# Performance work log

Measured on AMD Instinct MI355X. Metric: run time of the kernel, lower is better.

## Reference

```python
import jax, jax.numpy as jnp
import numpy as np

N = 50000
E = 800000
IN_DIM = 128
HID = 32
HEADS = 4
NEG_SLOPE = 0.2


def setup_inputs() -> dict:
    key = jax.random.key(0)
    ks = jax.random.split(key, 12)
    x = jax.random.normal(ks[0], (N, IN_DIM), dtype=jnp.float32)
    edge_index = jax.random.randint(ks[1], (2, E), 0, N, dtype=jnp.int64)
    s1 = 1.0 / np.sqrt(IN_DIM)
    s2 = 1.0 / np.sqrt(HEADS * HID)
    W1 = jax.random.normal(ks[2], (IN_DIM, HEADS * HID), dtype=jnp.float32) * s1
    a_src1 = jax.random.normal(ks[3], (HEADS, HID), dtype=jnp.float32) * s1
    a_dst1 = jax.random.normal(ks[4], (HEADS, HID), dtype=jnp.float32) * s1
    b1 = jnp.zeros((HEADS * HID,), dtype=jnp.float32)
    W2 = jax.random.normal(ks[5], (HEADS * HID, HID), dtype=jnp.float32) * s2
    a_src2 = jax.random.normal(ks[6], (1, HID), dtype=jnp.float32) * s2
    a_dst2 = jax.random.normal(ks[7], (1, HID), dtype=jnp.float32) * s2
    b2 = jnp.zeros((HID,), dtype=jnp.float32)
    return {"x": x, "edge_index": edge_index, "W1": W1, "a_src1": a_src1,
            "a_dst1": a_dst1, "b1": b1, "W2": W2, "a_src2": a_src2,
            "a_dst2": a_dst2, "b2": b2}


def _gat_layer(x, W, a_src, a_dst, bias, src, dst, heads, ch):
    n = x.shape[0]
    h = (x @ W).reshape(n, heads, ch)                    # [N,H,C]
    # per-node attention halves (GATv1): a_src . h_i, a_dst . h_j
    al_s = jnp.einsum('nhc,hc->nh', h, a_src)            # [N,H]
    al_d = jnp.einsum('nhc,hc->nh', h, a_dst)
    e = jax.nn.leaky_relu(al_s[src] + al_d[dst], NEG_SLOPE)  # [E,H]
    # segment softmax over edges sharing the same destination
    e_max = jax.ops.segment_max(e, dst, num_segments=n)
    e_exp = jnp.exp(e - e_max[dst])
    denom = jax.ops.segment_sum(e_exp, dst, num_segments=n)
    alpha = e_exp / (denom[dst] + 1e-16)                 # [E,H]
    msg = h[src] * alpha[:, :, None]                     # [E,H,C]
    out = jax.ops.segment_sum(msg, dst, num_segments=n)  # [N,H,C]
    return out.reshape(n, heads * ch) + bias


def reference(x, edge_index, W1, a_src1, a_dst1, b1, W2, a_src2, a_dst2, b2):
    n = x.shape[0]
    # PyG GATConv adds self-loops by default
    loops = jnp.arange(n, dtype=edge_index.dtype)
    src = jnp.concatenate([edge_index[0], loops])
    dst = jnp.concatenate([edge_index[1], loops])
    h = _gat_layer(x, W1, a_src1, a_dst1, b1, src, dst, HEADS, HID)
    h = jax.nn.elu(h)
    out = _gat_layer(h, W2, a_src2, a_dst2, b2, src, dst, 1, HID)
    return out
```

## Files before the change

### kernel.cpp

```cpp
#include <hip/hip_runtime.h>
#include <hip/hip_bf16.h>

#define NN 50000
#define EE 800000
#define EN (EE + NN)
#define IN_DIM 128
#define HID 32
#define HEADS 4
#define F1 (HEADS * HID)
#define NEG 0.2f
#define SLOT 64
#define CPAD 16

typedef __hip_bfloat16 bf16;
typedef __bf16 bf16x8 __attribute__((ext_vector_type(8)));
typedef float f32x4 __attribute__((ext_vector_type(4)));

__device__ __forceinline__ float cvt(float v) { return v; }
__device__ __forceinline__ float cvt(bf16 v)  { return __bfloat162float(v); }

__device__ __forceinline__ float bflo(unsigned u) {
    union { unsigned u; float f; } v; v.u = u << 16; return v.f;
}
__device__ __forceinline__ float bfhi(unsigned u) {
    union { unsigned u; float f; } v; v.u = u & 0xFFFF0000u; return v.f;
}

__device__ __forceinline__ unsigned short f2bf_bits(float f) {
    union { float f; unsigned u; } v; v.f = f;
    unsigned r = v.u + 0x7FFFu + ((v.u >> 16) & 1u);
    return (unsigned short)(r >> 16);
}

__device__ __forceinline__ unsigned short f2h_bits(float f) {
    _Float16 h = (_Float16)f;
    union { _Float16 h; unsigned short s; } v; v.h = h; return v.s;
}
__device__ __forceinline__ float h2f(unsigned short s) {
    union { _Float16 h; unsigned short s; } v; v.s = s; return (float)v.h;
}

#define ZERO_B ((NN * CPAD + 255) / 256)
#define PREP_B (1 + ZERO_B + 16 + 1)

__global__ void k_prep(const void* xv, const void* eiv,
                       const void* W1v, const void* W2v,
                       int* __restrict__ flags, int* __restrict__ counts,
                       unsigned short* __restrict__ W1T,
                       unsigned short* __restrict__ W2T) {
    const int b = blockIdx.x, t = threadIdx.x;
    if (b == 0) {
        if (t < 64) {
            const unsigned* xw = (const unsigned*)xv;
            const unsigned* ew = (const unsigned*)eiv;
            int lo_nz = 0, huge = 0, hi_nz = 0;
            for (int j = 0; j < 4; ++j) {
                unsigned w = xw[t * 4 + j];
                unsigned lo = w & 0xFFFFu;
                if (lo != 0u) lo_nz = 1;
                if (((lo >> 7) & 0xFFu) >= 0xC0u) huge = 1;
                unsigned eo = ew[(t * 4 + j) * 2 + 1];
                if (eo != 0u) hi_nz = 1;
            }
            unsigned long long m_lo = __ballot(lo_nz);
            unsigned long long m_hg = __ballot(huge);
            unsigned long long m_hi = __ballot(hi_nz);
            if (t == 0) {
                flags[0] = (m_lo == 0ull || m_hg != 0ull) ? 1 : 0;
                flags[1] = (m_hi == 0ull) ? 1 : 0;
            }
        }
        return;
    }
    if (b <= ZERO_B) {
        int i = (b - 1) * 256 + t;
        if (i < NN * CPAD) counts[i] = 0;
        return;
    }
    __shared__ int sf;
    if (t < 64) {
        const unsigned* xw = (const unsigned*)xv;
        int lo_nz = 0, huge = 0;
        for (int j = 0; j < 4; ++j) {
            unsigned w = xw[t * 4 + j];
            unsigned lo = w & 0xFFFFu;
            if (lo != 0u) lo_nz = 1;
            if (((lo >> 7) & 0xFFu) >= 0xC0u) huge = 1;
        }
        unsigned long long m_lo = __ballot(lo_nz);
        unsigned long long m_hg = __ballot(huge);
        if (t == 0) sf = (m_lo == 0ull || m_hg != 0ull) ? 1 : 0;
    }
    __syncthreads();
    const int f32in = sf;
    const int tb = b - 1 - ZERO_B;
    if (tb < 16) {
        const unsigned short* wg = (const unsigned short*)W1v;
        const float* wf = (const float*)W1v;
        for (int i = 0; i < 4; ++i) {
            int j = tb * 1024 + i * 256 + t;
            int k = j >> 7, n = j & 127;
            W1T[n * 128 + k] = f32in ? f2bf_bits(wf[j]) : wg[j];
        }
    } else {
        const unsigned short* wg = (const unsigned short*)W2v;
        const float* wf = (const float*)W2v;
        for (int i = 0; i < 16; ++i) {
            int j = i * 256 + t;
            int k = j >> 5, n = j & 31;
            W2T[n * 128 + k] = f32in ? f2bf_bits(wf[j]) : wg[j];
        }
    }
}

#define PAIR_B ((EN / 2 + 255) / 256)

__global__ void k_hist(const void* ei, const int* __restrict__ flags,
                       int* __restrict__ counts, int* __restrict__ sr) {
    int p = blockIdx.x * 256 + threadIdx.x;
    int i2 = p * 2;
    if (i2 >= EN) return;
    int s0, s1, d0, d1;
    if (i2 >= EE) { s0 = d0 = i2 - EE; s1 = d1 = s0 + 1; }
    else if (flags[1]) {
        const long long* e64 = (const long long*)ei;
        long2 ss = *(const long2*)&e64[i2];
        long2 dd = *(const long2*)&e64[EE + i2];
        s0 = (int)ss.x; s1 = (int)ss.y; d0 = (int)dd.x; d1 = (int)dd.y;
    } else {
        const int* e32 = (const int*)ei;
        int2 ss = *(const int2*)&e32[i2];
        int2 dd = *(const int2*)&e32[EE + i2];
        s0 = ss.x; s1 = ss.y; d0 = dd.x; d1 = dd.y;
    }
    int r0 = atomicAdd(&counts[d0 * CPAD], 1);
    int r1 = atomicAdd(&counts[d1 * CPAD], 1);
    int slot0 = (r0 < SLOT) ? d0 * SLOT + r0 : -1;
    int slot1 = (r1 < SLOT) ? d1 * SLOT + r1 : -1;
    *(int4*)&sr[i2 * 2] = make_int4(slot0, s0, slot1, s1);
}

#define MROWS 64
#define LDK 136
#define LIN_B ((NN + MROWS - 1) / MROWS)
#define FUSE_B (LIN_B + PAIR_B)

__global__ __launch_bounds__(256) void k_fused(
    const void* xv, const unsigned short* __restrict__ W1T,
    const void* as1v, const void* ad1v,
    const int* __restrict__ flags, const int* __restrict__ sr,
    int* __restrict__ srcs2, unsigned* __restrict__ h1,
    float* __restrict__ als, float* __restrict__ ald)
{
    if (blockIdx.x >= LIN_B) {
        int p = (blockIdx.x - LIN_B) * 256 + threadIdx.x;
        int i2 = p * 2;
        if (i2 >= EN) return;
        int4 v = *(const int4*)&sr[i2 * 2];
        if (v.x >= 0) srcs2[v.x] = v.y;
        if (v.z >= 0) srcs2[v.z] = v.w;
        return;
    }

    __shared__ __align__(16) char smem[(MROWS + 128) * LDK * 2];
    unsigned short* xs  = (unsigned short*)smem;
    unsigned short* w1t = xs + MROWS * LDK;
    float* hs = (float*)smem;
    __shared__ float sa[F1], sd[F1];

    const int t = threadIdx.x;
    const int row0 = blockIdx.x * MROWS;
    const int f32in = flags[0];

    if (t < F1) {
        sa[t] = f32in ? ((const float*)as1v)[t] : cvt(((const bf16*)as1v)[t]);
        sd[t] = f32in ? ((const float*)ad1v)[t] : cvt(((const bf16*)ad1v)[t]);
    }
    if (!f32in) {
        const uint4* xg = (const uint4*)xv;
        for (int i = 0; i < 4; ++i) {
            int id = i * 256 + t;
            int m = id >> 4, seg = id & 15;
            int gr = row0 + m;
            uint4 val = (gr < NN) ? xg[(size_t)gr * 16 + seg] : make_uint4(0, 0, 0, 0);
            *(uint4*)&xs[m * LDK + seg * 8] = val;
        }
    } else {
        const float4* xf = (const float4*)xv;
        for (int i = 0; i < 8; ++i) {
            int id = i * 256 + t;
            int m = id >> 5, c = id & 31;
            int gr = row0 + m;
            float4 v = (gr < NN) ? xf[(size_t)gr * 32 + c]
                                 : make_float4(0.f, 0.f, 0.f, 0.f);
            unsigned w0 = (unsigned)f2bf_bits(v.x) | ((unsigned)f2bf_bits(v.y) << 16);
            unsigned w1 = (unsigned)f2bf_bits(v.z) | ((unsigned)f2bf_bits(v.w) << 16);
            *(uint2*)&xs[m * LDK + c * 4] = make_uint2(w0, w1);
        }
    }
    {
        const uint4* wg = (const uint4*)W1T;
        for (int i = 0; i < 8; ++i) {
            int id = i * 256 + t;
            int n = id >> 4, seg = id & 15;
            *(uint4*)&w1t[n * LDK + seg * 8] = wg[id];
        }
    }
    __syncthreads();

    const int wave = t >> 6, lane = t & 63, quad = lane >> 4, l16 = lane & 15;
    f32x4 acc[8];
#pragma unroll
    for (int ni = 0; ni < 8; ++ni) acc[ni] = (f32x4){0.f, 0.f, 0.f, 0.f};

    const int arow = wave * 16 + l16;
#pragma unroll
    for (int kc = 0; kc < 4; ++kc) {
        int ko = kc * 32 + quad * 8;
        bf16x8 av = *(const bf16x8*)&xs[arow * LDK + ko];
#pragma unroll
        for (int ni = 0; ni < 8; ++ni) {
            bf16x8 bv = *(const bf16x8*)&w1t[(ni * 16 + l16) * LDK + ko];
            acc[ni] = __builtin_amdgcn_mfma_f32_16x16x32_bf16(av, bv, acc[ni], 0, 0, 0);
        }
    }
    __syncthreads();

#pragma unroll
    for (int ni = 0; ni < 8; ++ni)
#pragma unroll
        for (int r = 0; r < 4; ++r) {
            int m = wave * 16 + quad * 4 + r;
            hs[m * 132 + ni * 16 + l16] = acc[ni][r];
        }
    __syncthreads();

    for (int i = 0; i < 16; ++i) {
        int id = i * 256 + t;
        int m = id >> 6, wd = id & 63;
        int gr = row0 + m;
        if (gr < NN) {
            unsigned pw = (unsigned)f2bf_bits(hs[m * 132 + 2 * wd]) |
                          ((unsigned)f2bf_bits(hs[m * 132 + 2 * wd + 1]) << 16);
            h1[(size_t)gr * 64 + wd] = pw;
        }
    }
    {
        int m = t >> 2, h = t & 3;
        int gr = row0 + m;
        if (gr < NN) {
            float ps = 0.f, pd = 0.f;
#pragma unroll
            for (int jj = 0; jj < 32; ++jj) {
                int j = (jj + 8 * h) & 31;
                float v = hs[m * 132 + h * 32 + j];
                ps += v * sa[h * 32 + j];
                pd += v * sd[h * 32 + j];
            }
            als[gr * 4 + h] = ps;
            ald[gr * 4 + h] = pd;
        }
    }
}

__global__ __launch_bounds__(256) void k_agg1(
    const int* __restrict__ counts, const int* __restrict__ srcs2,
    const float* __restrict__ als, const float* __restrict__ ald,
    const bf16* __restrict__ h1, const void* b1v, const int* __restrict__ flags,
    uint4* __restrict__ hm)
{
    const int lane = threadIdx.x & 63;
    const int d = blockIdx.x * 4 + (threadIdx.x >> 6);
    const int q = lane >> 4;
    const int u = lane & 15;
    const int h = u >> 2;
    const int start = d * SLOT;
    const int end = start + min(counts[d * CPAD], SLOT);
    const uint4* rows = (const uint4*)h1;
    const float advh = ald[d * 4 + h];

    float A[8] = {0,0,0,0,0,0,0,0}, B[8] = {0,0,0,0,0,0,0,0};
    float DA = 0.f, DB = 0.f;
    int e = start + q;
    for (; e + 4 < end; e += 8) {
        int s0 = srcs2[e], s1 = srcs2[e + 4];
        float e0 = als[s0 * 4 + h] + advh;
        float e1 = als[s1 * 4 + h] + advh;
        e0 = e0 > 0.f ? e0 : NEG * e0;
        e1 = e1 > 0.f ? e1 : NEG * e1;
        float x0 = __expf(e0), x1 = __expf(e1);
        uint4 u0 = rows[(size_t)s0 * 16 + u];
        uint4 u1 = rows[(size_t)s1 * 16 + u];
        A[0] += x0 * bflo(u0.x); A[1] += x0 * bfhi(u0.x);
        A[2] += x0 * bflo(u0.y); A[3] += x0 * bfhi(u0.y);
        A[4] += x0 * bflo(u0.z); A[5] += x0 * bfhi(u0.z);
        A[6] += x0 * bflo(u0.w); A[7] += x0 * bfhi(u0.w); DA += x0;
        B[0] += x1 * bflo(u1.x); B[1] += x1 * bfhi(u1.x);
        B[2] += x1 * bflo(u1.y); B[3] += x1 * bfhi(u1.y);
        B[4] += x1 * bflo(u1.z); B[5] += x1 * bfhi(u1.z);
        B[6] += x1 * bflo(u1.w); B[7] += x1 * bfhi(u1.w); DB += x1;
    }
    for (; e < end; e += 4) {
        int s0 = srcs2[e];
        float e0 = als[s0 * 4 + h] + advh;
        e0 = e0 > 0.f ? e0 : NEG * e0;
        float x0 = __expf(e0);
        uint4 u0 = rows[(size_t)s0 * 16 + u];
        A[0] += x0 * bflo(u0.x); A[1] += x0 * bfhi(u0.x);
        A[2] += x0 * bflo(u0.y); A[3] += x0 * bfhi(u0.y);
        A[4] += x0 * bflo(u0.z); A[5] += x0 * bfhi(u0.z);
        A[6] += x0 * bflo(u0.w); A[7] += x0 * bfhi(u0.w); DA += x0;
    }
    float a[8];
#pragma unroll
    for (int j = 0; j < 8; ++j) a[j] = A[j] + B[j];
    float dsum = DA + DB;
#pragma unroll
    for (int j = 0; j < 8; ++j) {
        a[j] += __shfl_xor(a[j], 16);
        a[j] += __shfl_xor(a[j], 32);
    }
    dsum += __shfl_xor(dsum, 16);
    dsum += __shfl_xor(dsum, 32);
    if (q == 0) {
        float inv = 1.f / (dsum + 1e-16f);
        float bb[8];
        if (flags[0]) {
            float4 b0 = ((const float4*)b1v)[2 * u];
            float4 b1 = ((const float4*)b1v)[2 * u + 1];
            bb[0] = b0.x; bb[1] = b0.y; bb[2] = b0.z; bb[3] = b0.w;
            bb[4] = b1.x; bb[5] = b1.y; bb[6] = b1.z; bb[7] = b1.w;
        } else {
            uint4 ub = ((const uint4*)b1v)[u];
            bb[0] = bflo(ub.x); bb[1] = bfhi(ub.x); bb[2] = bflo(ub.y); bb[3] = bfhi(ub.y);
            bb[4] = bflo(ub.z); bb[5] = bfhi(ub.z); bb[6] = bflo(ub.w); bb[7] = bfhi(ub.w);
        }
        float v[8];
#pragma unroll
        for (int j = 0; j < 8; ++j) {
            float vv = a[j] * inv + bb[j];
            v[j] = vv > 0.f ? vv : (__expf(vv) - 1.f);
        }
        uint4 w;
        w.x = (unsigned)f2bf_bits(v[0]) | ((unsigned)f2bf_bits(v[1]) << 16);
        w.y = (unsigned)f2bf_bits(v[2]) | ((unsigned)f2bf_bits(v[3]) << 16);
        w.z = (unsigned)f2bf_bits(v[4]) | ((unsigned)f2bf_bits(v[5]) << 16);
        w.w = (unsigned)f2bf_bits(v[6]) | ((unsigned)f2bf_bits(v[7]) << 16);
        hm[(size_t)d * 16 + u] = w;
    }
}

__global__ __launch_bounds__(256) void k_mid_mfma(
    const bf16* __restrict__ hm, const unsigned short* __restrict__ W2T,
    const void* as2v, const void* ad2v,
    const int* __restrict__ flags, unsigned short* __restrict__ h2,
    float* __restrict__ als2, float* __restrict__ ald2)
{
    __shared__ __align__(16) unsigned short hs[MROWS * LDK];
    __shared__ __align__(16) unsigned short w2t[32 * LDK];
    __shared__ float sa2[HID], sd2[HID];

    const int t = threadIdx.x;
    const int row0 = blockIdx.x * MROWS;
    const int f32in = flags[0];

    if (t < HID) {
        sa2[t] = f32in ? ((const float*)as2v)[t] : cvt(((const bf16*)as2v)[t]);
        sd2[t] = f32in ? ((const float*)ad2v)[t] : cvt(((const bf16*)ad2v)[t]);
    }
    {
        const uint4* hg = (const uint4*)hm;
        for (int i = 0; i < 4; ++i) {
            int id = i * 256 + t;
            int m = id >> 4, seg = id & 15;
            int gr = row0 + m;
            uint4 val = (gr < NN) ? hg[(size_t)gr * 16 + seg] : make_uint4(0, 0, 0, 0);
            *(uint4*)&hs[m * LDK + seg * 8] = val;
        }
        const uint4* wg = (const uint4*)W2T;
        for (int i = 0; i < 2; ++i) {
            int id = i * 256 + t;
            int n = id >> 4, seg = id & 15;
            *(uint4*)&w2t[n * LDK + seg * 8] = wg[id];
        }
    }
    __syncthreads();

    const int wave = t >> 6, lane = t & 63, quad = lane >> 4, l16 = lane & 15;
    f32x4 acc[2];
    acc[0] = (f32x4){0.f, 0.f, 0.f, 0.f};
    acc[1] = (f32x4){0.f, 0.f, 0.f, 0.f};
    const int arow = wave * 16 + l16;
#pragma unroll
    for (int kc = 0; kc < 4; ++kc) {
        int ko = kc * 32 + quad * 8;
        bf16x8 av = *(const bf16x8*)&hs[arow * LDK + ko];
#pragma unroll
        for (int ni = 0; ni < 2; ++ni) {
            bf16x8 bv = *(const bf16x8*)&w2t[(ni * 16 + l16) * LDK + ko];
            acc[ni] = __builtin_amdgcn_mfma_f32_16x16x32_bf16(av, bv, acc[ni], 0, 0, 0);
        }
    }

#pragma unroll
    for (int ni = 0; ni < 2; ++ni)
#pragma unroll
        for (int r = 0; r < 4; ++r) {
            int gr = row0 + wave * 16 + quad * 4 + r;
            if (gr < NN) h2[(size_t)gr * 32 + ni * 16 + l16] = f2h_bits(acc[ni][r]);
        }

    float ps[4], pd[4];
#pragma unroll
    for (int r = 0; r < 4; ++r) {
        ps[r] = acc[0][r] * sa2[l16] + acc[1][r] * sa2[16 + l16];
        pd[r] = acc[0][r] * sd2[l16] + acc[1][r] * sd2[16 + l16];
    }
#pragma unroll
    for (int mask = 1; mask < 16; mask <<= 1)
#pragma unroll
        for (int r = 0; r < 4; ++r) {
            ps[r] += __shfl_xor(ps[r], mask);
            pd[r] += __shfl_xor(pd[r], mask);
        }
    if (l16 == 0) {
#pragma unroll
        for (int r = 0; r < 4; ++r) {
            int gr = row0 + wave * 16 + quad * 4 + r;
            if (gr < NN) { als2[gr] = ps[r]; ald2[gr] = pd[r]; }
        }
    }
}

__global__ __launch_bounds__(256) void k_agg2(
    const int* __restrict__ counts, const int* __restrict__ srcs2,
    const float* __restrict__ als2, const float* __restrict__ ald2,
    const uint2* __restrict__ h2,
    const void* b2v, const int* __restrict__ flags, void* out)
{
    const int lane = threadIdx.x & 63;
    const int node = blockIdx.x * 4 + (threadIdx.x >> 6);
    const int q = lane >> 3;
    const int u = lane & 7;
    const int start = node * SLOT;
    const int end = start + min(counts[node * CPAD], SLOT);
    const float adv = ald2[node];

    float A0 = 0.f, A1 = 0.f, A2 = 0.f, A3 = 0.f, D0 = 0.f;
    for (int e = start + q; e < end; e += 8) {
        int s0 = srcs2[e];
        float e0 = als2[s0] + adv;
        e0 = e0 > 0.f ? e0 : NEG * e0;
        float x0 = __expf(e0);
        uint2 w = h2[(size_t)s0 * 8 + u];
        A0 += x0 * h2f((unsigned short)(w.x & 0xFFFFu));
        A1 += x0 * h2f((unsigned short)(w.x >> 16));
        A2 += x0 * h2f((unsigned short)(w.y & 0xFFFFu));
        A3 += x0 * h2f((unsigned short)(w.y >> 16));
        D0 += x0;
    }
    A0 += __shfl_xor(A0, 8);  A1 += __shfl_xor(A1, 8);
    A2 += __shfl_xor(A2, 8);  A3 += __shfl_xor(A3, 8);  D0 += __shfl_xor(D0, 8);
    A0 += __shfl_xor(A0, 16); A1 += __shfl_xor(A1, 16);
    A2 += __shfl_xor(A2, 16); A3 += __shfl_xor(A3, 16); D0 += __shfl_xor(D0, 16);
    A0 += __shfl_xor(A0, 32); A1 += __shfl_xor(A1, 32);
    A2 += __shfl_xor(A2, 32); A3 += __shfl_xor(A3, 32); D0 += __shfl_xor(D0, 32);
    if (q == 0) {
        float inv = 1.f / (D0 + 1e-16f);
        float r0 = A0 * inv, r1 = A1 * inv, r2 = A2 * inv, r3 = A3 * inv;
        if (flags[0]) {
            float4 bb = ((const float4*)b2v)[u];
            ((float4*)out)[(size_t)node * 8 + u] =
                make_float4(r0 + bb.x, r1 + bb.y, r2 + bb.z, r3 + bb.w);
        } else {
            uint2 ub = ((const uint2*)b2v)[u];
            r0 += bflo(ub.x); r1 += bfhi(ub.x); r2 += bflo(ub.y); r3 += bfhi(ub.y);
            unsigned w0 = (unsigned)f2bf_bits(r0) | ((unsigned)f2bf_bits(r1) << 16);
            unsigned w1 = (unsigned)f2bf_bits(r2) | ((unsigned)f2bf_bits(r3) << 16);
            ((uint2*)out)[(size_t)node * 8 + u] = make_uint2(w0, w1);
        }
    }
}

extern "C" void kernel_launch(void* const* d_in, const int* in_sizes, int n_in,
                              void* d_out, int out_size, void* d_ws, size_t ws_size,
                              hipStream_t stream) {
    const void* x    = d_in[0];
    const void* ei   = d_in[1];
    const void* W1   = d_in[2];
    const void* a_s1 = d_in[3];
    const void* a_d1 = d_in[4];
    const void* b1   = d_in[5];
    const void* W2   = d_in[6];
    const void* a_s2 = d_in[7];
    const void* a_d2 = d_in[8];
    const void* b2v  = d_in[9];

    int*   flags  = (int*)d_ws;
    char*  pc     = (char*)d_ws + 256;
    uint4* hm     = (uint4*)pc;            pc += (size_t)NN * 16 * 16;
    int*   sr     = (int*)hm;
    bf16*  h1     = (bf16*)pc;             pc += (size_t)NN * F1 * 2;
    unsigned short* h2 = (unsigned short*)h1;
    int*   srcs2  = (int*)pc;              pc += (size_t)NN * SLOT * 4;
    float* al_s1  = (float*)pc;            pc += (size_t)NN * HEADS * 4;
    float* al_d1  = (float*)pc;            pc += (size_t)NN * HEADS * 4;
    float* al_s2  = (float*)pc;            pc += (size_t)NN * 4;
    float* al_d2  = (float*)pc;            pc += (size_t)NN * 4;
    int*   counts = (int*)pc;              pc += (size_t)NN * CPAD * 4;
    unsigned short* W1T = (unsigned short*)pc; pc += (size_t)128 * 128 * 2;
    unsigned short* W2T = (unsigned short*)pc; pc += (size_t)32 * 128 * 2;

    k_prep<<<PREP_B, 256, 0, stream>>>(x, ei, W1, W2, flags, counts, W1T, W2T);
    k_hist<<<PAIR_B, 256, 0, stream>>>(ei, flags, counts, sr);
    k_fused<<<FUSE_B, 256, 0, stream>>>(x, W1T, a_s1, a_d1, flags, sr, srcs2,
                                        (unsigned*)h1, al_s1, al_d1);
    k_agg1<<<NN / 4, 256, 0, stream>>>(counts, srcs2, al_s1, al_d1, h1, b1,
                                       flags, hm);
    k_mid_mfma<<<(NN + MROWS - 1) / MROWS, 256, 0, stream>>>((const bf16*)hm, W2T, a_s2,
                                                             a_d2, flags, h2, al_s2, al_d2);
    k_agg2<<<NN / 4, 256, 0, stream>>>(counts, srcs2, al_s2, al_d2,
                                       (const uint2*)h2, b2v, flags, d_out);
}
```

Measured before the change: 214.7 us.

## Fuse layer-2 linear projection and attention logits into layer-1 aggregation kernel

Removes the separate MFMA mid kernel. After each wave finishes aggregating a node's layer-1 features and applying bias and ELU, it stages the 128-wide row in shared memory and computes the 32-wide W2 projection with scalar FMAs, plus the layer-2 attention logits. This avoids writing and re-reading the intermediate hm buffer and saves a launch. In exchange, every wave reloads W2T from cache and does non-tensor-core math, and the workspace layout changes so h2 and sr no longer alias.

```diff
diff --git a/kernel.cpp b/kernel.cpp
--- a/kernel.cpp
+++ b/kernel.cpp
@@ -266,11 +266,17 @@
 __global__ __launch_bounds__(256) void k_agg1(
     const int* __restrict__ counts, const int* __restrict__ srcs2,
     const float* __restrict__ als, const float* __restrict__ ald,
-    const bf16* __restrict__ h1, const void* b1v, const int* __restrict__ flags,
-    uint4* __restrict__ hm)
+    const bf16* __restrict__ h1, const void* b1v,
+    const unsigned short* __restrict__ W2T,
+    const void* as2v, const void* ad2v,
+    const int* __restrict__ flags,
+    unsigned short* __restrict__ h2,
+    float* __restrict__ als2, float* __restrict__ ald2)
 {
+    __shared__ float hmrow[4][128];
     const int lane = threadIdx.x & 63;
-    const int d = blockIdx.x * 4 + (threadIdx.x >> 6);
+    const int wave = threadIdx.x >> 6;
+    const int d = blockIdx.x * 4 + wave;
     const int q = lane >> 4;
     const int u = lane & 15;
     const int h = u >> 2;
@@ -322,114 +328,54 @@
     }
     dsum += __shfl_xor(dsum, 16);
     dsum += __shfl_xor(dsum, 32);
+
+    float inv = 1.f / (dsum + 1e-16f);
+    float bb[8];
+    if (flags[0]) {
+        float4 b0 = ((const float4*)b1v)[2 * u];
+        float4 b1 = ((const float4*)b1v)[2 * u + 1];
+        bb[0] = b0.x; bb[1] = b0.y; bb[2] = b0.z; bb[3] = b0.w;
+        bb[4] = b1.x; bb[5] = b1.y; bb[6] = b1.z; bb[7] = b1.w;
+    } else {
+        uint4 ub = ((const uint4*)b1v)[u];
+        bb[0] = bflo(ub.x); bb[1] = bfhi(ub.x); bb[2] = bflo(ub.y); bb[3] = bfhi(ub.y);
+        bb[4] = bflo(ub.z); bb[5] = bfhi(ub.z); bb[6] = bflo(ub.w); bb[7] = bfhi(ub.w);
+    }
+    float v[8];
+#pragma unroll
+    for (int j = 0; j < 8; ++j) {
+        float vv = a[j] * inv + bb[j];
+        v[j] = vv > 0.f ? vv : (__expf(vv) - 1.f);
+    }
     if (q == 0) {
-        float inv = 1.f / (dsum + 1e-16f);
-        float bb[8];
-        if (flags[0]) {
-            float4 b0 = ((const float4*)b1v)[2 * u];
-            float4 b1 = ((const float4*)b1v)[2 * u + 1];
-            bb[0] = b0.x; bb[1] = b0.y; bb[2] = b0.z; bb[3] = b0.w;
-            bb[4] = b1.x; bb[5] = b1.y; bb[6] = b1.z; bb[7] = b1.w;
-        } else {
-            uint4 ub = ((const uint4*)b1v)[u];
-            bb[0] = bflo(ub.x); bb[1] = bfhi(ub.x); bb[2] = bflo(ub.y); bb[3] = bfhi(ub.y);
-            bb[4] = bflo(ub.z); bb[5] = bfhi(ub.z); bb[6] = bflo(ub.w); bb[7] = bfhi(ub.w);
-        }
-        float v[8];
-#pragma unroll
-        for (int j = 0; j < 8; ++j) {
-            float vv = a[j] * inv + bb[j];
-            v[j] = vv > 0.f ? vv : (__expf(vv) - 1.f);
-        }
-        uint4 w;
-        w.x = (unsigned)f2bf_bits(v[0]) | ((unsigned)f2bf_bits(v[1]) << 16);
-        w.y = (unsigned)f2bf_bits(v[2]) | ((unsigned)f2bf_bits(v[3]) << 16);
-        w.z = (unsigned)f2bf_bits(v[4]) | ((unsigned)f2bf_bits(v[5]) << 16);
-        w.w = (unsigned)f2bf_bits(v[6]) | ((unsigned)f2bf_bits(v[7]) << 16);
-        hm[(size_t)d * 16 + u] = w;
-    }
-}
-
-__global__ __launch_bounds__(256) void k_mid_mfma(
-    const bf16* __restrict__ hm, const unsigned short* __restrict__ W2T,
-    const void* as2v, const void* ad2v,
-    const int* __restrict__ flags, unsigned short* __restrict__ h2,
-    float* __restrict__ als2, float* __restrict__ ald2)
-{
-    __shared__ __align__(16) unsigned short hs[MROWS * LDK];
-    __shared__ __align__(16) unsigned short w2t[32 * LDK];
-    __shared__ float sa2[HID], sd2[HID];
-
-    const int t = threadIdx.x;
-    const int row0 = blockIdx.x * MROWS;
-    const int f32in = flags[0];
-
-    if (t < HID) {
-        sa2[t] = f32in ? ((const float*)as2v)[t] : cvt(((const bf16*)as2v)[t]);
-        sd2[t] = f32in ? ((const float*)ad2v)[t] : cvt(((const bf16*)ad2v)[t]);
-    }
-    {
-        const uint4* hg = (const uint4*)hm;
-        for (int i = 0; i < 4; ++i) {
-            int id = i * 256 + t;
-            int m = id >> 4, seg = id & 15;
-            int gr = row0 + m;
-            uint4 val = (gr < NN) ? hg[(size_t)gr * 16 + seg] : make_uint4(0, 0, 0, 0);
-            *(uint4*)&hs[m * LDK + seg * 8] = val;
-        }
-        const uint4* wg = (const uint4*)W2T;
-        for (int i = 0; i < 2; ++i) {
-            int id = i * 256 + t;
-            int n = id >> 4, seg = id & 15;
-            *(uint4*)&w2t[n * LDK + seg * 8] = wg[id];
-        }
-    }
-    __syncthreads();
-
-    const int wave = t >> 6, lane = t & 63, quad = lane >> 4, l16 = lane & 15;
-    f32x4 acc[2];
-    acc[0] = (f32x4){0.f, 0.f, 0.f, 0.f};
-    acc[1] = (f32x4){0.f, 0.f, 0.f, 0.f};
-    const int arow = wave * 16 + l16;
-#pragma unroll
-    for (int kc = 0; kc < 4; ++kc) {
-        int ko = kc * 32 + quad * 8;
-        bf16x8 av = *(const bf16x8*)&hs[arow * LDK + ko];
-#pragma unroll
-        for (int ni = 0; ni < 2; ++ni) {
-            bf16x8 bv = *(const bf16x8*)&w2t[(ni * 16 + l16) * LDK + ko];
-            acc[ni] = __builtin_amdgcn_mfma_f32_16x16x32_bf16(av, bv, acc[ni], 0, 0, 0);
-        }
-    }
-
-#pragma unroll
-    for (int ni = 0; ni < 2; ++ni)
-#pragma unroll
-        for (int r = 0; r < 4; ++r) {
-            int gr = row0 + wave * 16 + quad * 4 + r;
-            if (gr < NN) h2[(size_t)gr * 32 + ni * 16 + l16] = f2h_bits(acc[ni][r]);
-        }
-
-    float ps[4], pd[4];
-#pragma unroll
-    for (int r = 0; r < 4; ++r) {
-        ps[r] = acc[0][r] * sa2[l16] + acc[1][r] * sa2[16 + l16];
-        pd[r] = acc[0][r] * sd2[l16] + acc[1][r] * sd2[16 + l16];
-    }
-#pragma unroll
-    for (int mask = 1; mask < 16; mask <<= 1)
-#pragma unroll
-        for (int r = 0; r < 4; ++r) {
-            ps[r] += __shfl_xor(ps[r], mask);
-            pd[r] += __shfl_xor(pd[r], mask);
-        }
-    if (l16 == 0) {
-#pragma unroll
-        for (int r = 0; r < 4; ++r) {
-            int gr = row0 + wave * 16 + quad * 4 + r;
-            if (gr < NN) { als2[gr] = ps[r]; ald2[gr] = pd[r]; }
-        }
-    }
+#pragma unroll
+        for (int j = 0; j < 8; ++j) hmrow[wave][u * 8 + j] = v[j];
+    }
+    const int n = lane & 31, half = lane >> 5;
+    const uint4* w2g = (const uint4*)W2T;
+    uint4 w2r[8];
+#pragma unroll
+    for (int j = 0; j < 8; ++j) w2r[j] = w2g[n * 16 + half * 8 + j];
+    float acc2 = 0.f;
+#pragma unroll
+    for (int j = 0; j < 8; ++j) {
+        const float* hr = &hmrow[wave][half * 64 + j * 8];
+        acc2 += hr[0] * bflo(w2r[j].x) + hr[1] * bfhi(w2r[j].x)
+              + hr[2] * bflo(w2r[j].y) + hr[3] * bfhi(w2r[j].y)
+              + hr[4] * bflo(w2r[j].z) + hr[5] * bfhi(w2r[j].z)
+              + hr[6] * bflo(w2r[j].w) + hr[7] * bfhi(w2r[j].w);
+    }
+    acc2 += __shfl_xor(acc2, 32);
+    float sa2n = flags[0] ? ((const float*)as2v)[n] : cvt(((const bf16*)as2v)[n]);
+    float sd2n = flags[0] ? ((const float*)ad2v)[n] : cvt(((const bf16*)ad2v)[n]);
+    float ps = acc2 * sa2n, pd = acc2 * sd2n;
+#pragma unroll
+    for (int mask = 1; mask < 32; mask <<= 1) {
+        ps += __shfl_xor(ps, mask);
+        pd += __shfl_xor(pd, mask);
+    }
+    if (lane < 32) h2[(size_t)d * 32 + n] = f2h_bits(acc2);
+    if (lane == 0) { als2[d] = ps; ald2[d] = pd; }
 }
 
 __global__ __launch_bounds__(256) void k_agg2(
@@ -498,10 +444,9 @@
 
     int*   flags  = (int*)d_ws;
     char*  pc     = (char*)d_ws + 256;
-    uint4* hm     = (uint4*)pc;            pc += (size_t)NN * 16 * 16;
-    int*   sr     = (int*)hm;
+    int*   sr     = (int*)pc;              pc += (size_t)EN * 16;
     bf16*  h1     = (bf16*)pc;             pc += (size_t)NN * F1 * 2;
-    unsigned short* h2 = (unsigned short*)h1;
+    unsigned short* h2 = (unsigned short*)pc; pc += (size_t)NN * HID * 2;
     int*   srcs2  = (int*)pc;              pc += (size_t)NN * SLOT * 4;
     float* al_s1  = (float*)pc;            pc += (size_t)NN * HEADS * 4;
     float* al_d1  = (float*)pc;            pc += (size_t)NN * HEADS * 4;
@@ -516,9 +461,8 @@
     k_fused<<<FUSE_B, 256, 0, stream>>>(x, W1T, a_s1, a_d1, flags, sr, srcs2,
                                         (unsigned*)h1, al_s1, al_d1);
     k_agg1<<<NN / 4, 256, 0, stream>>>(counts, srcs2, al_s1, al_d1, h1, b1,
-                                       flags, hm);
-    k_mid_mfma<<<(NN + MROWS - 1) / MROWS, 256, 0, stream>>>((const bf16*)hm, W2T, a_s2,
-                                                             a_d2, flags, h2, al_s2, al_d2);
+                                       W2T, a_s2, a_d2, flags,
+                                       h2, al_s2, al_d2);
     k_agg2<<<NN / 4, 256, 0, stream>>>(counts, srcs2, al_s2, al_d2,
                                        (const uint2*)h2, b2v, flags, d_out);
 }
```

New measurement: 240.4 us. +12.0%, slower.

## Overlap edge histogram with layer-1 GEMM; read W1 from global, epilogue from registers

Applied to the files above, without the earlier changes.

Moves the edge-count histogram (atomic slot assignment) into the fused GEMM kernel's extra blocks and turns the scatter of source indices into a separate small kernel, so the histogram runs alongside the layer-1 projection instead of in its own launch. The GEMM no longer stages W1 into shared memory and reads B fragments straight from global/L2. Its epilogue writes bf16 h1 and computes the attention dot-products directly from MFMA accumulators with lane shuffles, dropping the shared-memory round trip and two barriers. The trade-offs are scattered 2-byte global stores for h1 and more global traffic for W1 reads.

```diff
diff --git a/kernel.cpp b/kernel.cpp
--- a/kernel.cpp
+++ b/kernel.cpp
@@ -113,59 +113,46 @@
     }
 }
 
-#define PAIR_B ((EN / 2 + 255) / 256)
-
-__global__ void k_hist(const void* ei, const int* __restrict__ flags,
-                       int* __restrict__ counts, int* __restrict__ sr) {
-    int p = blockIdx.x * 256 + threadIdx.x;
-    int i2 = p * 2;
-    if (i2 >= EN) return;
-    int s0, s1, d0, d1;
-    if (i2 >= EE) { s0 = d0 = i2 - EE; s1 = d1 = s0 + 1; }
-    else if (flags[1]) {
-        const long long* e64 = (const long long*)ei;
-        long2 ss = *(const long2*)&e64[i2];
-        long2 dd = *(const long2*)&e64[EE + i2];
-        s0 = (int)ss.x; s1 = (int)ss.y; d0 = (int)dd.x; d1 = (int)dd.y;
-    } else {
-        const int* e32 = (const int*)ei;
-        int2 ss = *(const int2*)&e32[i2];
-        int2 dd = *(const int2*)&e32[EE + i2];
-        s0 = ss.x; s1 = ss.y; d0 = dd.x; d1 = dd.y;
-    }
-    int r0 = atomicAdd(&counts[d0 * CPAD], 1);
-    int r1 = atomicAdd(&counts[d1 * CPAD], 1);
-    int slot0 = (r0 < SLOT) ? d0 * SLOT + r0 : -1;
-    int slot1 = (r1 < SLOT) ? d1 * SLOT + r1 : -1;
-    *(int4*)&sr[i2 * 2] = make_int4(slot0, s0, slot1, s1);
-}
-
 #define MROWS 64
 #define LDK 136
 #define LIN_B ((NN + MROWS - 1) / MROWS)
+#define PAIR_B ((EN / 2 + 255) / 256)
 #define FUSE_B (LIN_B + PAIR_B)
 
 __global__ __launch_bounds__(256) void k_fused(
-    const void* xv, const unsigned short* __restrict__ W1T,
+    const void* xv, const void* eiv, const unsigned short* __restrict__ W1T,
     const void* as1v, const void* ad1v,
-    const int* __restrict__ flags, const int* __restrict__ sr,
-    int* __restrict__ srcs2, unsigned* __restrict__ h1,
+    const int* __restrict__ flags,
+    int* __restrict__ counts, int* __restrict__ sr,
+    unsigned short* __restrict__ h1s,
     float* __restrict__ als, float* __restrict__ ald)
 {
     if (blockIdx.x >= LIN_B) {
         int p = (blockIdx.x - LIN_B) * 256 + threadIdx.x;
         int i2 = p * 2;
         if (i2 >= EN) return;
-        int4 v = *(const int4*)&sr[i2 * 2];
-        if (v.x >= 0) srcs2[v.x] = v.y;
-        if (v.z >= 0) srcs2[v.z] = v.w;
+        int s0, s1, d0, d1;
+        if (i2 >= EE) { s0 = d0 = i2 - EE; s1 = d1 = s0 + 1; }
+        else if (flags[1]) {
+            const long long* e64 = (const long long*)eiv;
+            long2 ss = *(const long2*)&e64[i2];
+            long2 dd = *(const long2*)&e64[EE + i2];
+            s0 = (int)ss.x; s1 = (int)ss.y; d0 = (int)dd.x; d1 = (int)dd.y;
+        } else {
+            const int* e32 = (const int*)eiv;
+            int2 ss = *(const int2*)&e32[i2];
+            int2 dd = *(const int2*)&e32[EE + i2];
+            s0 = ss.x; s1 = ss.y; d0 = dd.x; d1 = dd.y;
+        }
+        int r0 = atomicAdd(&counts[d0 * CPAD], 1);
+        int r1 = atomicAdd(&counts[d1 * CPAD], 1);
+        int slot0 = (r0 < SLOT) ? d0 * SLOT + r0 : -1;
+        int slot1 = (r1 < SLOT) ? d1 * SLOT + r1 : -1;
+        *(int4*)&sr[i2 * 2] = make_int4(slot0, s0, slot1, s1);
         return;
     }
 
-    __shared__ __align__(16) char smem[(MROWS + 128) * LDK * 2];
-    unsigned short* xs  = (unsigned short*)smem;
-    unsigned short* w1t = xs + MROWS * LDK;
-    float* hs = (float*)smem;
+    __shared__ __align__(16) unsigned short xs[MROWS * LDK];
     __shared__ float sa[F1], sd[F1];
 
     const int t = threadIdx.x;
@@ -198,14 +185,6 @@
             *(uint2*)&xs[m * LDK + c * 4] = make_uint2(w0, w1);
         }
     }
-    {
-        const uint4* wg = (const uint4*)W1T;
-        for (int i = 0; i < 8; ++i) {
-            int id = i * 256 + t;
-            int n = id >> 4, seg = id & 15;
-            *(uint4*)&w1t[n * LDK + seg * 8] = wg[id];
-        }
-    }
     __syncthreads();
 
     const int wave = t >> 6, lane = t & 63, quad = lane >> 4, l16 = lane & 15;
@@ -220,47 +199,53 @@
         bf16x8 av = *(const bf16x8*)&xs[arow * LDK + ko];
 #pragma unroll
         for (int ni = 0; ni < 8; ++ni) {
-            bf16x8 bv = *(const bf16x8*)&w1t[(ni * 16 + l16) * LDK + ko];
+            bf16x8 bv = *(const bf16x8*)&W1T[(ni * 16 + l16) * 128 + ko];
             acc[ni] = __builtin_amdgcn_mfma_f32_16x16x32_bf16(av, bv, acc[ni], 0, 0, 0);
         }
     }
-    __syncthreads();
-
-#pragma unroll
-    for (int ni = 0; ni < 8; ++ni)
-#pragma unroll
-        for (int r = 0; r < 4; ++r) {
-            int m = wave * 16 + quad * 4 + r;
-            hs[m * 132 + ni * 16 + l16] = acc[ni][r];
-        }
-    __syncthreads();
-
-    for (int i = 0; i < 16; ++i) {
-        int id = i * 256 + t;
-        int m = id >> 6, wd = id & 63;
-        int gr = row0 + m;
+
+    const int gr0 = row0 + wave * 16 + quad * 4;
+#pragma unroll
+    for (int r = 0; r < 4; ++r) {
+        int gr = gr0 + r;
         if (gr < NN) {
-            unsigned pw = (unsigned)f2bf_bits(hs[m * 132 + 2 * wd]) |
-                          ((unsigned)f2bf_bits(hs[m * 132 + 2 * wd + 1]) << 16);
-            h1[(size_t)gr * 64 + wd] = pw;
-        }
-    }
-    {
-        int m = t >> 2, h = t & 3;
-        int gr = row0 + m;
-        if (gr < NN) {
-            float ps = 0.f, pd = 0.f;
-#pragma unroll
-            for (int jj = 0; jj < 32; ++jj) {
-                int j = (jj + 8 * h) & 31;
-                float v = hs[m * 132 + h * 32 + j];
-                ps += v * sa[h * 32 + j];
-                pd += v * sd[h * 32 + j];
+#pragma unroll
+            for (int ni = 0; ni < 8; ++ni)
+                h1s[(size_t)gr * 128 + ni * 16 + l16] = f2bf_bits(acc[ni][r]);
+        }
+    }
+#pragma unroll
+    for (int r = 0; r < 4; ++r) {
+        float ps[4], pd[4];
+#pragma unroll
+        for (int h = 0; h < 4; ++h) {
+            ps[h] = acc[2 * h][r]     * sa[h * 32 + l16]
+                  + acc[2 * h + 1][r] * sa[h * 32 + 16 + l16];
+            pd[h] = acc[2 * h][r]     * sd[h * 32 + l16]
+                  + acc[2 * h + 1][r] * sd[h * 32 + 16 + l16];
+        }
+#pragma unroll
+        for (int mask = 1; mask < 16; mask <<= 1)
+#pragma unroll
+            for (int h = 0; h < 4; ++h) {
+                ps[h] += __shfl_xor(ps[h], mask);
+                pd[h] += __shfl_xor(pd[h], mask);
             }
-            als[gr * 4 + h] = ps;
-            ald[gr * 4 + h] = pd;
-        }
-    }
+        int gr = gr0 + r;
+        if (l16 == 0 && gr < NN) {
+            *(float4*)&als[gr * 4] = make_float4(ps[0], ps[1], ps[2], ps[3]);
+            *(float4*)&ald[gr * 4] = make_float4(pd[0], pd[1], pd[2], pd[3]);
+        }
+    }
+}
+
+__global__ void k_scatter(const int* __restrict__ sr, int* __restrict__ srcs2) {
+    int p = blockIdx.x * 256 + threadIdx.x;
+    int i2 = p * 2;
+    if (i2 >= EN) return;
+    int4 v = *(const int4*)&sr[i2 * 2];
+    if (v.x >= 0) srcs2[v.x] = v.y;
+    if (v.z >= 0) srcs2[v.z] = v.w;
 }
 
 __global__ __launch_bounds__(256) void k_agg1(
@@ -512,9 +497,10 @@
     unsigned short* W2T = (unsigned short*)pc; pc += (size_t)32 * 128 * 2;
 
     k_prep<<<PREP_B, 256, 0, stream>>>(x, ei, W1, W2, flags, counts, W1T, W2T);
-    k_hist<<<PAIR_B, 256, 0, stream>>>(ei, flags, counts, sr);
-    k_fused<<<FUSE_B, 256, 0, stream>>>(x, W1T, a_s1, a_d1, flags, sr, srcs2,
-                                        (unsigned*)h1, al_s1, al_d1);
+    k_fused<<<FUSE_B, 256, 0, stream>>>(x, ei, W1T, a_s1, a_d1, flags,
+                                        counts, sr, (unsigned short*)h1,
+                                        al_s1, al_d1);
+    k_scatter<<<PAIR_B, 256, 0, stream>>>(sr, srcs2);
     k_agg1<<<NN / 4, 256, 0, stream>>>(counts, srcs2, al_s1, al_d1, h1, b1,
                                        flags, hm);
     k_mid_mfma<<<(NN + MROWS - 1) / MROWS, 256, 0, stream>>>((const bf16*)hm, W2T, a_s2,
```

New measurement: 209.5 us. -2.4%, faster.
